# Performance work log

Measured on AMD Instinct MI355X. Metric: run time of the kernel, lower is better.

The kernel has to match this reference:

```python
import jax, jax.numpy as jnp
import numpy as np

B, S, IN, OUT = 4, 2048, 4096, 4096


def setup_inputs() -> dict:
    key = jax.random.key(0)
    k1, k2 = jax.random.split(key, 2)
    x = jax.random.normal(k1, (B, S, IN), dtype=jnp.float32)
    # Materialize the quantized weight the way bitsandbytes int8_vectorwise_quant does:
    # per-output-row absmax (SCB) and int8 codes CB = round(W * 127 / absmax_row).
    Wf = jax.random.normal(k2, (OUT, IN), dtype=jnp.float32) * 0.02
    absmax = jnp.max(jnp.abs(Wf), axis=1)  # [OUT]
    CB = jnp.round(Wf * (127.0 / absmax)[:, None]).astype(jnp.int8)  # [OUT, IN]
    SCB = absmax.astype(jnp.float32)  # [OUT], per-row absmax scale
    return {"x": x, "CB": CB, "SCB": SCB}


def reference(x, CB, SCB):
    # LLM.int8()-style forward (has_fp16_weights=False, no outlier split needed for
    # well-behaved activations): dynamic row-wise int8 quantization of x, int8 GEMM
    # accumulated in int32, then dequant by (absmax_x/127) * (SCB/127).
    absmax_x = jnp.max(jnp.abs(x), axis=-1, keepdims=True)  # [B,S,1]
    sx = absmax_x / 127.0
    xq = jnp.round(x / sx).astype(jnp.int8)  # [B,S,IN]
    acc = jnp.einsum("bsk,ok->bso", xq, CB, preferred_element_type=jnp.int32)
    y = acc.astype(jnp.float32) * sx * (SCB / 127.0)[None, None, :]  # [B,S,OUT]
    return y
```

## Files before the change

kernel.cpp:

```cpp
#include <hip/hip_runtime.h>
#include <stdint.h>

static constexpr int Mtot = 8192;
static constexpr int Ntot = 4096;
static constexpr int Ktot = 4096;

using i32x4 = __attribute__((ext_vector_type(4))) int;

#define GLD16(gptr, lptr)                                                                   \
  __builtin_amdgcn_global_load_lds((const __attribute__((address_space(1))) void*)(gptr),   \
                                   (__attribute__((address_space(3))) void*)(lptr), 16, 0, 0)

__global__ __launch_bounds__(256) void pack_cb_kernel(const int* __restrict__ src,
                                                      int8_t* __restrict__ dst) {
  const int idx = blockIdx.x * 256 + threadIdx.x;
  const int4 v = reinterpret_cast<const int4*>(src)[idx];
  const unsigned packed = (unsigned)(v.x & 0xff) | ((unsigned)(v.y & 0xff) << 8) |
                          ((unsigned)(v.z & 0xff) << 16) | ((unsigned)(v.w & 0xff) << 24);
  reinterpret_cast<unsigned*>(dst)[idx] = packed;
}

__global__ __launch_bounds__(256) void quant_x_kernel(const float* __restrict__ x,
                                                      int8_t* __restrict__ xq,
                                                      float* __restrict__ sx) {
  const int row = blockIdx.x;
  const float4* xr = reinterpret_cast<const float4*>(x + (size_t)row * Ktot);
  float4 v[4];
  float am = 0.f;
#pragma unroll
  for (int i = 0; i < 4; ++i) {
    v[i] = xr[threadIdx.x + i * 256];
    am = fmaxf(am, fmaxf(fmaxf(fabsf(v[i].x), fabsf(v[i].y)),
                         fmaxf(fabsf(v[i].z), fabsf(v[i].w))));
  }
#pragma unroll
  for (int off = 32; off > 0; off >>= 1) am = fmaxf(am, __shfl_xor(am, off));
  __shared__ float wmax[4];
  if ((threadIdx.x & 63) == 0) wmax[threadIdx.x >> 6] = am;
  __syncthreads();
  am = fmaxf(fmaxf(wmax[0], wmax[1]), fmaxf(wmax[2], wmax[3]));
  const float inv = 127.0f / am;
  if (threadIdx.x == 0) sx[row] = am * (1.0f / 127.0f);
  unsigned* dq = reinterpret_cast<unsigned*>(xq + (size_t)row * Ktot);
#pragma unroll
  for (int i = 0; i < 4; ++i) {
    const int q0 = (int)rintf(v[i].x * inv);
    const int q1 = (int)rintf(v[i].y * inv);
    const int q2 = (int)rintf(v[i].z * inv);
    const int q3 = (int)rintf(v[i].w * inv);
    dq[threadIdx.x + i * 256] = (unsigned)(q0 & 0xff) | ((unsigned)(q1 & 0xff) << 8) |
                                ((unsigned)(q2 & 0xff) << 16) | ((unsigned)(q3 & 0xff) << 24);
  }
}

__global__ __launch_bounds__(256) void gemm_i8_kernel(const int8_t* __restrict__ A,
                                                      const int8_t* __restrict__ B,
                                                      const float* __restrict__ sx,
                                                      const float* __restrict__ scb,
                                                      float* __restrict__ C) {
  constexpr int BK = 64;
  __shared__ int8_t As[128 * BK];
  __shared__ int8_t Bs[128 * BK];

  const int tid = threadIdx.x;
  const int lane = tid & 63;
  const int wid = tid >> 6;
  const int m0 = blockIdx.y * 128;
  const int n0 = blockIdx.x * 128;
  const int wm = (wid >> 1) * 64;
  const int wn = (wid & 1) * 64;

  const int srow = tid >> 2;
  const int scol = (tid & 3) * 16;
  const int8_t* Ag0 = A + (size_t)(m0 + srow) * Ktot + scol;
  const int8_t* Ag1 = A + (size_t)(m0 + 64 + srow) * Ktot + scol;
  const int8_t* Bg0 = B + (size_t)(n0 + srow) * Ktot + scol;
  const int8_t* Bg1 = B + (size_t)(n0 + 64 + srow) * Ktot + scol;
  int8_t* lA0 = &As[tid * 16];
  int8_t* lA1 = &As[4096 + tid * 16];
  int8_t* lB0 = &Bs[tid * 16];
  int8_t* lB1 = &Bs[4096 + tid * 16];

  i32x4 acc[4][4];
#pragma unroll
  for (int i = 0; i < 4; ++i)
#pragma unroll
    for (int j = 0; j < 4; ++j) acc[i][j] = (i32x4)0;

  const int mrow = lane & 15;
  const int kq = (lane >> 4) * 16;

  for (int kt = 0; kt < Ktot; kt += BK) {
    GLD16(Ag0 + kt, lA0);
    GLD16(Ag1 + kt, lA1);
    GLD16(Bg0 + kt, lB0);
    GLD16(Bg1 + kt, lB1);
    __syncthreads();

    i32x4 af[4], bf[4];
#pragma unroll
    for (int i = 0; i < 4; ++i)
      af[i] = *reinterpret_cast<const i32x4*>(&As[(wm + i * 16 + mrow) * BK + kq]);
#pragma unroll
    for (int j = 0; j < 4; ++j)
      bf[j] = *reinterpret_cast<const i32x4*>(&Bs[(wn + j * 16 + mrow) * BK + kq]);
#pragma unroll
    for (int i = 0; i < 4; ++i)
#pragma unroll
      for (int j = 0; j < 4; ++j)
        acc[i][j] = __builtin_amdgcn_mfma_i32_16x16x64_i8(af[i], bf[j], acc[i][j], 0, 0, 0);
    __syncthreads();
  }

  const int col = lane & 15;
  const int rbase = (lane >> 4) * 4;
#pragma unroll
  for (int i = 0; i < 4; ++i) {
    const int gmb = m0 + wm + i * 16 + rbase;
    float sm[4];
#pragma unroll
    for (int r = 0; r < 4; ++r) sm[r] = sx[gmb + r];
#pragma unroll
    for (int j = 0; j < 4; ++j) {
      const int gn = n0 + wn + j * 16 + col;
      const float snv = scb[gn] * (1.0f / 127.0f);
#pragma unroll
      for (int r = 0; r < 4; ++r)
        C[(size_t)(gmb + r) * Ntot + gn] = (float)acc[i][j][r] * sm[r] * snv;
    }
  }
}

extern "C" void kernel_launch(void* const* d_in, const int* in_sizes, int n_in,
                              void* d_out, int out_size, void* d_ws, size_t ws_size,
                              hipStream_t stream) {
  const float* x = (const float*)d_in[0];
  const int* CB32 = (const int*)d_in[1];
  const float* SCB = (const float*)d_in[2];
  float* out = (float*)d_out;

  int8_t* xq = (int8_t*)d_ws;
  int8_t* cb8 = (int8_t*)d_ws + (size_t)Mtot * Ktot;
  float* sx = (float*)((int8_t*)d_ws + (size_t)Mtot * Ktot + (size_t)Ntot * Ktot);

  pack_cb_kernel<<<(Ntot * Ktot / 4) / 256, 256, 0, stream>>>(CB32, cb8);
  quant_x_kernel<<<Mtot, 256, 0, stream>>>(x, xq, sx);
  dim3 grid(Ntot / 128, Mtot / 128);
  gemm_i8_kernel<<<grid, 256, 0, stream>>>(xq, cb8, sx, SCB, out);
}
```

Measured before the change: 418.7 us.

## Switch GEMM to 32x32x32 int8 MFMA with XOR-swizzled LDS layout

Replaces the 16x16x64 int8 MFMA tiling (16 instructions per K-step) with 32x32x32 MFMAs arranged 2x2 per wave, issued twice per 64-wide K tile. The aim is fewer LDS fragment loads and better MFMA throughput per byte read. The global-to-LDS column placement is XOR-swizzled by row so that fragment reads avoid LDS bank conflicts, and the read offsets are precomputed to match. The epilogue is remapped to the 32x32 accumulator layout, which gives a different store pattern.

New measurement: 445.2 us. 6.3% more time.

```diff
diff --git a/kernel.cpp b/kernel.cpp
--- a/kernel.cpp
+++ b/kernel.cpp
@@ -5,7 +5,8 @@
 static constexpr int Ntot = 4096;
 static constexpr int Ktot = 4096;
 
-using i32x4 = __attribute__((ext_vector_type(4))) int;
+using i32x4  = __attribute__((ext_vector_type(4)))  int;
+using i32x16 = __attribute__((ext_vector_type(16))) int;
 
 #define GLD16(gptr, lptr)                                                                   \
   __builtin_amdgcn_global_load_lds((const __attribute__((address_space(1))) void*)(gptr),   \
@@ -71,7 +72,7 @@
   const int wn = (wid & 1) * 64;
 
   const int srow = tid >> 2;
-  const int scol = (tid & 3) * 16;
+  const int scol = (((tid & 3) ^ ((srow >> 1) & 3)) << 4);
   const int8_t* Ag0 = A + (size_t)(m0 + srow) * Ktot + scol;
   const int8_t* Ag1 = A + (size_t)(m0 + 64 + srow) * Ktot + scol;
   const int8_t* Bg0 = B + (size_t)(n0 + srow) * Ktot + scol;
@@ -81,14 +82,29 @@
   int8_t* lB0 = &Bs[tid * 16];
   int8_t* lB1 = &Bs[4096 + tid * 16];
 
-  i32x4 acc[4][4];
+  i32x16 acc[2][2];
 #pragma unroll
-  for (int i = 0; i < 4; ++i)
+  for (int i = 0; i < 2; ++i)
 #pragma unroll
-    for (int j = 0; j < 4; ++j) acc[i][j] = (i32x4)0;
+    for (int j = 0; j < 2; ++j) acc[i][j] = (i32x16)0;
 
-  const int mrow = lane & 15;
-  const int kq = (lane >> 4) * 16;
+  const int mr = lane & 31;
+  const int kh = lane >> 5;
+  int offA[2][2], offB[2][2];
+#pragma unroll
+  for (int i = 0; i < 2; ++i) {
+    const int r = wm + i * 32 + mr;
+    const int sw = (r >> 1) & 3;
+#pragma unroll
+    for (int s = 0; s < 2; ++s) offA[i][s] = r * 64 + ((((s << 1) + kh) ^ sw) << 4);
+  }
+#pragma unroll
+  for (int j = 0; j < 2; ++j) {
+    const int r = wn + j * 32 + mr;
+    const int sw = (r >> 1) & 3;
+#pragma unroll
+    for (int s = 0; s < 2; ++s) offB[j][s] = r * 64 + ((((s << 1) + kh) ^ sw) << 4);
+  }
 
   for (int kt = 0; kt < Ktot; kt += BK) {
     GLD16(Ag0 + kt, lA0);
@@ -97,36 +113,38 @@
     GLD16(Bg1 + kt, lB1);
     __syncthreads();
 
-    i32x4 af[4], bf[4];
 #pragma unroll
-    for (int i = 0; i < 4; ++i)
-      af[i] = *reinterpret_cast<const i32x4*>(&As[(wm + i * 16 + mrow) * BK + kq]);
-#pragma unroll
-    for (int j = 0; j < 4; ++j)
-      bf[j] = *reinterpret_cast<const i32x4*>(&Bs[(wn + j * 16 + mrow) * BK + kq]);
-#pragma unroll
-    for (int i = 0; i < 4; ++i)
-#pragma unroll
-      for (int j = 0; j < 4; ++j)
-        acc[i][j] = __builtin_amdgcn_mfma_i32_16x16x64_i8(af[i], bf[j], acc[i][j], 0, 0, 0);
+    for (int s = 0; s < 2; ++s) {
+      const i32x4 a0 = *reinterpret_cast<const i32x4*>(&As[offA[0][s]]);
+      const i32x4 a1 = *reinterpret_cast<const i32x4*>(&As[offA[1][s]]);
+      const i32x4 b0 = *reinterpret_cast<const i32x4*>(&Bs[offB[0][s]]);
+      const i32x4 b1 = *reinterpret_cast<const i32x4*>(&Bs[offB[1][s]]);
+      acc[0][0] = __builtin_amdgcn_mfma_i32_32x32x32_i8(a0, b0, acc[0][0], 0, 0, 0);
+      acc[0][1] = __builtin_amdgcn_mfma_i32_32x32x32_i8(a0, b1, acc[0][1], 0, 0, 0);
+      acc[1][0] = __builtin_amdgcn_mfma_i32_32x32x32_i8(a1, b0, acc[1][0], 0, 0, 0);
+      acc[1][1] = __builtin_amdgcn_mfma_i32_32x32x32_i8(a1, b1, acc[1][1], 0, 0, 0);
+    }
     __syncthreads();
   }
 
-  const int col = lane & 15;
-  const int rbase = (lane >> 4) * 4;
+  const int col = lane & 31;
+  const int rq = (lane >> 5) << 2;
 #pragma unroll
-  for (int i = 0; i < 4; ++i) {
-    const int gmb = m0 + wm + i * 16 + rbase;
-    float sm[4];
+  for (int i = 0; i < 2; ++i) {
+    const int gmb = m0 + wm + i * 32;
+    float sm[16];
 #pragma unroll
-    for (int r = 0; r < 4; ++r) sm[r] = sx[gmb + r];
+    for (int reg = 0; reg < 16; ++reg)
+      sm[reg] = sx[gmb + (reg & 3) + ((reg >> 2) << 3) + rq];
 #pragma unroll
-    for (int j = 0; j < 4; ++j) {
-      const int gn = n0 + wn + j * 16 + col;
+    for (int j = 0; j < 2; ++j) {
+      const int gn = n0 + wn + j * 32 + col;
       const float snv = scb[gn] * (1.0f / 127.0f);
 #pragma unroll
-      for (int r = 0; r < 4; ++r)
-        C[(size_t)(gmb + r) * Ntot + gn] = (float)acc[i][j][r] * sm[r] * snv;
+      for (int reg = 0; reg < 16; ++reg) {
+        const int gm = gmb + (reg & 3) + ((reg >> 2) << 3) + rq;
+        C[(size_t)gm * Ntot + gn] = (float)acc[i][j][reg] * sm[reg] * snv;
+      }
     }
   }
 }
```
